# Kernel tuning notes

Measured on AMD Instinct MI355X. Metric: run time of the kernel, lower is better.

Reference implementation:

```python
import jax, jax.numpy as jnp
import numpy as np
from jax import lax

HIDDEN_CH = 32
KS = 3


def _conv(x, w):
    # x: [B, Cin, H, W], w: [Cout, Cin, k, k] -> [B, Cout, H, W] (SAME padding)
    return lax.conv_general_dilated(
        x, w, window_strides=(1, 1), padding='SAME',
        dimension_numbers=('NCHW', 'OIHW', 'NCHW'))


def _cell(x, h, gw, gb, cw, cb):
    combined = jnp.concatenate([x, h], axis=1)
    gates = jax.nn.sigmoid(_conv(combined, gw) + gb[None, :, None, None])
    r, z = jnp.split(gates, 2, axis=1)
    combined_r = jnp.concatenate([x, r * h], axis=1)
    n = jnp.tanh(_conv(combined_r, cw) + cb[None, :, None, None])
    return (1.0 - z) * h + z * n


def setup_inputs() -> dict:
    key = jax.random.key(0)
    ks = jax.random.split(key, 9)
    B, T, H, W = 8, 16, 128, 128
    hc = HIDDEN_CH
    seq = jax.random.normal(ks[0], (B, T, H, W), dtype=jnp.float32)

    def conv_init(k, cout, cin):
        fan_in = cin * KS * KS
        bound = 1.0 / np.sqrt(fan_in)
        return jax.random.uniform(k, (cout, cin, KS, KS), jnp.float32, -bound, bound)

    def bias_init(k, cout, cin):
        bound = 1.0 / np.sqrt(cin * KS * KS)
        return jax.random.uniform(k, (cout,), jnp.float32, -bound, bound)

    # Layer 0: input_ch=1, layer 1: input_ch=hc
    gw0 = conv_init(ks[1], 2 * hc, 1 + hc)
    gb0 = bias_init(ks[2], 2 * hc, 1 + hc)
    cw0 = conv_init(ks[3], hc, 1 + hc)
    cb0 = bias_init(ks[4], hc, 1 + hc)
    gw1 = conv_init(ks[5], 2 * hc, hc + hc)
    gb1 = bias_init(ks[6], 2 * hc, hc + hc)
    cw1 = conv_init(ks[7], hc, hc + hc)
    cb1 = bias_init(ks[8], hc, hc + hc)
    return {'seq': seq, 'gw0': gw0, 'gb0': gb0, 'cw0': cw0, 'cb0': cb0,
            'gw1': gw1, 'gb1': gb1, 'cw1': cw1, 'cb1': cb1}


def reference(seq, gw0, gb0, cw0, cb0, gw1, gb1, cw1, cb1):
    B, T, H, W = seq.shape
    hc = HIDDEN_CH
    h0 = jnp.zeros((B, hc, H, W), dtype=seq.dtype)
    h1 = jnp.zeros((B, hc, H, W), dtype=seq.dtype)
    # xs: [T, B, 1, H, W]
    xs = jnp.transpose(seq, (1, 0, 2, 3))[:, :, None, :, :]

    def step(carry, x_t):
        h0, h1 = carry
        h0 = _cell(x_t, h0, gw0, gb0, cw0, cb0)
        h1 = _cell(h0, h1, gw1, gb1, cw1, cb1)
        return (h0, h1), None

    (h0, h1), _ = lax.scan(step, (h0, h1), xs)
    return h1
```

## Files before the change

### kernel.cpp

```cpp
#include <hip/hip_runtime.h>


#define HH 128
#define PH 130
#define HW 16384
#define BB 8
#define TT 16

typedef _Float16 f16x8 __attribute__((ext_vector_type(8)));
typedef float f32x4 __attribute__((ext_vector_type(4)));
typedef unsigned int u32x4 __attribute__((ext_vector_type(4)));

__device__ __forceinline__ unsigned short f2h(float x){
    return __builtin_bit_cast(unsigned short, (_Float16)x);
}
__device__ __forceinline__ float h2f(unsigned short u){
    return (float)__builtin_bit_cast(_Float16, u);
}
__device__ __forceinline__ f16x8 ld_frag(const unsigned short* p){
    u32x4 v = *(const u32x4*)p;
    return __builtin_bit_cast(f16x8, v);
}
__device__ __forceinline__ f16x8 lds_frag_w(const unsigned short* base, int spix, int q){
    u32x4 v = *(const u32x4*)(base + spix * 32 + q * 8);
    return __builtin_bit_cast(f16x8, v);
}
__device__ __forceinline__ float sigmoid_f(float a){ return 1.0f / (1.0f + __expf(-a)); }
__device__ __forceinline__ float tanh_f(float a){ float e2 = __expf(2.0f * a); return 1.0f - 2.0f / (e2 + 1.0f); }

struct SmemT {
    unsigned short hs[2][13824];
    unsigned short rh[10880];
    float xt[444];
};

__device__ __forceinline__ void halo_rc10(int s, int& gr, int& gc){
    s = s > 83 ? 83 : s;
    if (s < 34)      { gr = 0;            gc = s;      }
    else if (s < 68) { gr = 9;            gc = s - 34; }
    else if (s < 76) { gr = 1 + (s - 68); gc = 0;      }
    else             { gr = 1 + (s - 76); gc = 33;     }
}

__device__ __forceinline__ f16x8 x_im2col(const float* xt, int gr, int gc, int q){
    f16x8 v;
#pragma unroll
    for (int j = 0; j < 8; ++j) {
        int k = q * 8 + j;
        float f = 0.0f;
        if (k < 9) f = xt[(gr + k / 3) * 37 + gc + k % 3];
        v[j] = (_Float16)f;
    }
    return v;
}

__device__ __forceinline__ void stage_plane12(unsigned short* slot,
    const unsigned short* __restrict__ g, int b, int pr0, int pc0)
{
    const int wv = threadIdx.x >> 6, lane = threadIdx.x & 63;
    for (int k = wv; k < 27; k += 8) {
        int chunk = k * 64 + lane;
        int pix = chunk >> 2, part = chunk & 3;
        int r = pix / 36, c = pix - r * 36;
        int pr = pr0 + r; pr = pr < 0 ? 0 : (pr > 129 ? 129 : pr);
        int pc = pc0 + c; pc = pc < 0 ? 0 : (pc > 129 ? 129 : pc);
        const unsigned short* ga = g + ((long)((b * PH + pr) * PH + pc) * 32 + part * 8);
        __builtin_amdgcn_global_load_lds(
            (const __attribute__((address_space(1))) unsigned int*)ga,
            (__attribute__((address_space(3))) unsigned int*)(slot + k * 512),
            16, 0, 0);
    }
}

__device__ __forceinline__ void stage_x12(float* xt, const float* __restrict__ seq,
                                          int b, int t, int R0, int C0)
{
    if (threadIdx.x < 444) {
        int p = threadIdx.x;
        int r = p / 37, c = p - r * 37;
        int ir = R0 - 2 + r, ic = C0 - 2 + c;
        float v = 0.0f;
        if (ir >= 0 && ir < HH && ic >= 0 && ic < HH)
            v = seq[((long)b * TT + t) * HW + ir * HH + ic];
        xt[p] = v;
    }
}

__global__ void prep_w(const float* __restrict__ w, unsigned short* __restrict__ wf,
                       int CO, int CIT, int NSTEP, int xmode)
{
    int idx = blockIdx.x * 256 + threadIdx.x;
    int total = NSTEP * CO * 32;
    if (idx >= total) return;
    int kk = idx & 31;
    int t  = idx >> 5;
    int co = t % CO;
    int s  = t / CO;
    float v = 0.0f;
    if (xmode && s == NSTEP - 1) {
        if (kk < 9) v = w[(co * CIT + 0) * 9 + kk];
    } else {
        int tap = s % 9;
        int cin = (s / 9) * 32 + kk + (xmode ? 1 : 0);
        v = w[(co * CIT + cin) * 9 + tap];
    }
    wf[idx] = f2h(v);
}

template<int L, int EMIT>
__device__ __forceinline__ void cell_compute(SmemT& sm,
    unsigned short* __restrict__ Hout,
    const unsigned short* __restrict__ Wg, const float* __restrict__ bg,
    const unsigned short* __restrict__ Wc, const float* __restrict__ bc,
    float* __restrict__ out, int b, int R0, int C0)
{
    constexpr int KG = (L == 0) ? 10 : 18;
    constexpr int KC = (L == 0) ? 10 : 18;

    const int wv = threadIdx.x >> 6, lane = threadIdx.x & 63;
    const int m16 = lane & 15, q = lane >> 4;
    const unsigned short* hp = (L == 0) ? sm.hs[0] : sm.hs[1];

    const bool HASH = (wv >= 2);
    int hgr = 0, hgc = 0;
    halo_rc10((wv - 2) * 16 + m16, hgr, hgc);

    f32x4 gI[2][4];
    f32x4 gH[2];
#pragma unroll
    for (int ng = 0; ng < 4; ++ng) {
        float bv = bg[ng * 16 + m16];
#pragma unroll
        for (int mg = 0; mg < 2; ++mg) gI[mg][ng] = f32x4{bv, bv, bv, bv};
        if (ng < 2) gH[ng] = f32x4{bv, bv, bv, bv};
    }

    f16x8 Bc[4];
#pragma unroll
    for (int ng = 0; ng < 4; ++ng)
        Bc[ng] = ld_frag(Wg + (ng * 16 + m16) * 32 + q * 8);

#pragma unroll
    for (int s = 0; s < KG; ++s) {
        f16x8 Bn[4];
        if (s + 1 < KG) {
#pragma unroll
            for (int ng = 0; ng < 4; ++ng)
                Bn[ng] = ld_frag(Wg + ((s + 1) * 64 + ng * 16 + m16) * 32 + q * 8);
        }
        f16x8 AI[2], AH;
        if (L == 0 && s == 9) {
#pragma unroll
            for (int mg = 0; mg < 2; ++mg)
                AI[mg] = x_im2col(sm.xt, wv + 1, mg * 16 + 1 + m16, q);
            AH = x_im2col(sm.xt, hgr, hgc, q);
        } else {
            const int tap = (L == 0) ? s : (s % 9);
            const unsigned short* pl = (L == 1 && s >= 9) ? sm.hs[1] : sm.hs[0];
#pragma unroll
            for (int mg = 0; mg < 2; ++mg)
                AI[mg] = lds_frag_w(pl, (wv + 1 + tap / 3) * 36 + mg * 16 + 1 + m16 + tap % 3, q);
            AH = lds_frag_w(pl, (hgr + tap / 3) * 36 + hgc + tap % 3, q);
        }
#pragma unroll
        for (int mg = 0; mg < 2; ++mg)
#pragma unroll
            for (int ng = 0; ng < 4; ++ng)
                gI[mg][ng] = __builtin_amdgcn_mfma_f32_16x16x32_f16(AI[mg], Bc[ng], gI[mg][ng], 0, 0, 0);
        if (HASH) {
#pragma unroll
            for (int ng = 0; ng < 2; ++ng)
                gH[ng] = __builtin_amdgcn_mfma_f32_16x16x32_f16(AH, Bc[ng], gH[ng], 0, 0, 0);
        }
        if (s + 1 < KG) {
#pragma unroll
            for (int ng = 0; ng < 4; ++ng) Bc[ng] = Bn[ng];
        }
    }

    unsigned int zpk[2][4];
#pragma unroll
    for (int mg = 0; mg < 2; ++mg)
#pragma unroll
        for (int rg = 0; rg < 4; ++rg) {
            int gr = wv + 1, gc = mg * 16 + 1 + q * 4 + rg;
            zpk[mg][rg] = (unsigned int)f2h(sigmoid_f(gI[mg][2][rg]))
                        | ((unsigned int)f2h(sigmoid_f(gI[mg][3][rg])) << 16);
#pragma unroll
            for (int ng = 0; ng < 2; ++ng) {
                int n = ng * 16 + m16;
                float rv = sigmoid_f(gI[mg][ng][rg]);
                float hv = h2f(hp[((gr + 1) * 36 + gc + 1) * 32 + n]);
                sm.rh[(gr * 34 + gc) * 32 + n] = f2h(rv * hv);
            }
        }
    if (HASH) {
#pragma unroll
        for (int rg = 0; rg < 4; ++rg) {
            int gr, gc; halo_rc10((wv - 2) * 16 + q * 4 + rg, gr, gc);
#pragma unroll
            for (int ng = 0; ng < 2; ++ng) {
                int n = ng * 16 + m16;
                float rv = sigmoid_f(gH[ng][rg]);
                float hv = h2f(hp[((gr + 1) * 36 + gc + 1) * 32 + n]);
                sm.rh[(gr * 34 + gc) * 32 + n] = f2h(rv * hv);
            }
        }
    }
    __syncthreads();

    f32x4 cacc[2][2];
#pragma unroll
    for (int mg = 0; mg < 2; ++mg)
#pragma unroll
        for (int ng = 0; ng < 2; ++ng) {
            float bv = bc[ng * 16 + m16];
            cacc[mg][ng] = f32x4{bv, bv, bv, bv};
        }
    f16x8 Cc[2];
#pragma unroll
    for (int ng = 0; ng < 2; ++ng)
        Cc[ng] = ld_frag(Wc + (ng * 16 + m16) * 32 + q * 8);
#pragma unroll
    for (int s = 0; s < KC; ++s) {
        f16x8 Cn[2];
        if (s + 1 < KC) {
#pragma unroll
            for (int ng = 0; ng < 2; ++ng)
                Cn[ng] = ld_frag(Wc + ((s + 1) * 32 + ng * 16 + m16) * 32 + q * 8);
        }
        f16x8 A2[2];
        if (L == 0 && s == 9) {
#pragma unroll
            for (int mg = 0; mg < 2; ++mg)
                A2[mg] = x_im2col(sm.xt, wv + 1, mg * 16 + 1 + m16, q);
        } else if (L == 1 && s < 9) {
#pragma unroll
            for (int mg = 0; mg < 2; ++mg)
                A2[mg] = lds_frag_w(sm.hs[0], (wv + 1 + s / 3) * 36 + mg * 16 + m16 + 1 + s % 3, q);
        } else {
            const int tap = (L == 0) ? s : (s - 9);
#pragma unroll
            for (int mg = 0; mg < 2; ++mg)
                A2[mg] = lds_frag_w(sm.rh, (wv + tap / 3) * 34 + mg * 16 + m16 + tap % 3, q);
        }
#pragma unroll
        for (int mg = 0; mg < 2; ++mg)
#pragma unroll
            for (int ng = 0; ng < 2; ++ng)
                cacc[mg][ng] = __builtin_amdgcn_mfma_f32_16x16x32_f16(A2[mg], Cc[ng], cacc[mg][ng], 0, 0, 0);
        if (s + 1 < KC) {
#pragma unroll
            for (int ng = 0; ng < 2; ++ng) Cc[ng] = Cn[ng];
        }
    }

    unsigned short hvout[2][2][4];
#pragma unroll
    for (int mg = 0; mg < 2; ++mg)
#pragma unroll
        for (int ng = 0; ng < 2; ++ng)
#pragma unroll
            for (int rg = 0; rg < 4; ++rg) {
                int lcol = mg * 16 + q * 4 + rg;
                int n = ng * 16 + m16;
                float nv = tanh_f(cacc[mg][ng][rg]);
                float zz = h2f((unsigned short)(zpk[mg][rg] >> (ng * 16)));
                float ho = h2f(hp[((wv + 2) * 36 + lcol + 2) * 32 + n]);
                float hnew = (1.0f - zz) * ho + zz * nv;
                if (!EMIT) {
                    long psp = (long)(b * PH + R0 + wv + 1) * PH + (C0 + lcol + 1);
                    Hout[psp * 32 + n] = f2h(hnew);
                } else {
                    hvout[mg][ng][rg] = f2h(hnew);
                }
            }

    if (EMIT) {
        __syncthreads();
        unsigned short* scr = sm.rh;
#pragma unroll
        for (int mg = 0; mg < 2; ++mg)
#pragma unroll
            for (int ng = 0; ng < 2; ++ng)
#pragma unroll
                for (int rg = 0; rg < 4; ++rg)
                    scr[((wv * 32 + mg * 16 + q * 4 + rg) * 32) + ng * 16 + m16] = hvout[mg][ng][rg];
        __syncthreads();
        const int tid = threadIdx.x;
        const int rowid = tid >> 1, half = tid & 1;
        const int n = rowid >> 3, wr = rowid & 7;
        long obase = ((long)(b * 32 + n) * HH + (R0 + wr)) * HH + C0 + half * 16;
#pragma unroll
        for (int j = 0; j < 16; ++j)
            out[obase + j] = h2f(scr[(wr * 32 + half * 16 + j) * 32 + n]);
    }
}

__global__ __launch_bounds__(512, 4)
void cell_l0(const unsigned short* __restrict__ Hin, unsigned short* __restrict__ Hout,
             const float* __restrict__ seq, int t,
             const unsigned short* __restrict__ Wg, const float* __restrict__ bg,
             const unsigned short* __restrict__ Wc, const float* __restrict__ bc)
{
    __shared__ __align__(16) SmemT sm;
    const int wg = blockIdx.x;
    const int b = wg >> 6, tr = (wg >> 2) & 15, tc = wg & 3;
    const int R0 = tr * 8, C0 = tc * 32;
    stage_x12(sm.xt, seq, b, t, R0, C0);
    stage_plane12(sm.hs[0], Hin, b, R0 - 1, C0 - 1);
    __syncthreads();
    cell_compute<0, 0>(sm, Hout, Wg, bg, Wc, bc, (float*)0, b, R0, C0);
}

__global__ __launch_bounds__(512, 4)
void fused_pair(const unsigned short* __restrict__ h1r, unsigned short* __restrict__ h1w,
                const unsigned short* __restrict__ h0r, unsigned short* __restrict__ h0w,
                const float* __restrict__ seq, int tnext,
                const unsigned short* __restrict__ WG0, const float* __restrict__ gb0,
                const unsigned short* __restrict__ WC0, const float* __restrict__ cb0,
                const unsigned short* __restrict__ WG1, const float* __restrict__ gb1,
                const unsigned short* __restrict__ WC1, const float* __restrict__ cb1)
{
    __shared__ __align__(16) SmemT sm;
    const int wg = blockIdx.x;
    const int b = wg >> 6, tr = (wg >> 2) & 15, tc = wg & 3;
    const int R0 = tr * 8, C0 = tc * 32;
    stage_x12(sm.xt, seq, b, tnext, R0, C0);
    stage_plane12(sm.hs[0], h0r, b, R0 - 1, C0 - 1);
    stage_plane12(sm.hs[1], h1r, b, R0 - 1, C0 - 1);
    __syncthreads();
    cell_compute<1, 0>(sm, h1w, WG1, gb1, WC1, cb1, (float*)0, b, R0, C0);
    __syncthreads();
    cell_compute<0, 0>(sm, h0w, WG0, gb0, WC0, cb0, (float*)0, b, R0, C0);
}

__global__ __launch_bounds__(512, 4)
void cell_l1_emit(const unsigned short* __restrict__ Hin,
                  const unsigned short* __restrict__ Xin,
                  const unsigned short* __restrict__ Wg, const float* __restrict__ bg,
                  const unsigned short* __restrict__ Wc, const float* __restrict__ bc,
                  float* __restrict__ out)
{
    __shared__ __align__(16) SmemT sm;
    const int wg = blockIdx.x;
    const int b = wg >> 6, tr = (wg >> 2) & 15, tc = wg & 3;
    const int R0 = tr * 8, C0 = tc * 32;
    stage_plane12(sm.hs[0], Xin, b, R0 - 1, C0 - 1);
    stage_plane12(sm.hs[1], Hin, b, R0 - 1, C0 - 1);
    __syncthreads();
    cell_compute<1, 1>(sm, (unsigned short*)0, Wg, bg, Wc, bc, out, b, R0, C0);
}

extern "C" void kernel_launch(void* const* d_in, const int* in_sizes, int n_in,
                              void* d_out, int out_size, void* d_ws, size_t ws_size,
                              hipStream_t stream)
{
    const float* seq = (const float*)d_in[0];
    const float* gw0 = (const float*)d_in[1];
    const float* gb0 = (const float*)d_in[2];
    const float* cw0 = (const float*)d_in[3];
    const float* cb0 = (const float*)d_in[4];
    const float* gw1 = (const float*)d_in[5];
    const float* gb1 = (const float*)d_in[6];
    const float* cw1 = (const float*)d_in[7];
    const float* cb1 = (const float*)d_in[8];
    float* out = (float*)d_out;

    const size_t NSP = (size_t)BB * PH * PH * 32;

    char* p = (char*)d_ws;
    unsigned short* S0A = (unsigned short*)p; p += NSP * 2;
    unsigned short* S0B = (unsigned short*)p; p += NSP * 2;
    unsigned short* S1A = (unsigned short*)p; p += NSP * 2;
    unsigned short* S1B = (unsigned short*)p; p += NSP * 2;
    unsigned short* WG0 = (unsigned short*)p; p += 20480 * 2;
    unsigned short* WC0 = (unsigned short*)p; p += 10240 * 2;
    unsigned short* WG1 = (unsigned short*)p; p += 36864 * 2;
    unsigned short* WC1 = (unsigned short*)p; p += 18432 * 2;

    hipMemsetAsync(S0A, 0, 4 * NSP * 2, stream);

    prep_w<<<(10 * 64 * 32 + 255) / 256, 256, 0, stream>>>(gw0, WG0, 64, 33, 10, 1);
    prep_w<<<(10 * 32 * 32 + 255) / 256, 256, 0, stream>>>(cw0, WC0, 32, 33, 10, 1);
    prep_w<<<(18 * 64 * 32 + 255) / 256, 256, 0, stream>>>(gw1, WG1, 64, 64, 18, 0);
    prep_w<<<(18 * 32 * 32 + 255) / 256, 256, 0, stream>>>(cw1, WC1, 32, 64, 18, 0);

    dim3 grid(512, 1, 1), block(512);

    cell_l0<<<grid, block, 0, stream>>>(S0A, S0B, seq, 0, WG0, gb0, WC0, cb0);

    unsigned short *h0r = S0B, *h0w = S0A, *h1r = S1A, *h1w = S1B;
    for (int t = 0; t < TT - 1; ++t) {
        fused_pair<<<grid, block, 0, stream>>>(h1r, h1w, h0r, h0w, seq, t + 1,
                                               WG0, gb0, WC0, cb0,
                                               WG1, gb1, WC1, cb1);
        unsigned short* tmp;
        tmp = h0r; h0r = h0w; h0w = tmp;
        tmp = h1r; h1r = h1w; h1w = tmp;
    }
    cell_l1_emit<<<grid, block, 0, stream>>>(h1r, h0r, WG1, gb1, WC1, cb1, out);
}
```

Before: 1.005 ms.

## Split layer cells into separate blocks and swizzle LDS activation tiles

The fused per-step kernel used to run the layer-1 cell and then the layer-0 cell one after the other inside each block. It now launches a grid with a z dimension of 2, so one set of blocks computes layer 1 and another set computes layer 0 concurrently, doubling the number of blocks per launch. Separately, staged activation planes and the r*h buffer in shared memory now use an XOR swizzle on load and on every access, to reduce LDS bank conflicts on the 16-byte fragment reads. The layer-0 blocks now stage the h0 halo themselves, so the h0 plane is read twice from global memory.

```diff
diff --git a/kernel.cpp b/kernel.cpp
--- a/kernel.cpp
+++ b/kernel.cpp
@@ -21,8 +21,10 @@
     u32x4 v = *(const u32x4*)p;
     return __builtin_bit_cast(f16x8, v);
 }
-__device__ __forceinline__ f16x8 lds_frag_w(const unsigned short* base, int spix, int q){
-    u32x4 v = *(const u32x4*)(base + spix * 32 + q * 8);
+__device__ __forceinline__ int swzus(int i){ return i ^ (((i >> 6) & 7) << 3); }
+__device__ __forceinline__ f16x8 lds_frag_s(const unsigned short* base, int spix, int q){
+    int idx = swzus(spix * 32 + q * 8);
+    u32x4 v = *(const u32x4*)(base + idx);
     return __builtin_bit_cast(f16x8, v);
 }
 __device__ __forceinline__ float sigmoid_f(float a){ return 1.0f / (1.0f + __expf(-a)); }
@@ -59,8 +61,9 @@
 {
     const int wv = threadIdx.x >> 6, lane = threadIdx.x & 63;
     for (int k = wv; k < 27; k += 8) {
-        int chunk = k * 64 + lane;
-        int pix = chunk >> 2, part = chunk & 3;
+        int u = k * 64 + lane;
+        int cch = u ^ ((u >> 3) & 7);
+        int pix = cch >> 2, part = cch & 3;
         int r = pix / 36, c = pix - r * 36;
         int pr = pr0 + r; pr = pr < 0 ? 0 : (pr > 129 ? 129 : pr);
         int pc = pc0 + c; pc = pc < 0 ? 0 : (pc > 129 ? 129 : pc);
@@ -159,8 +162,8 @@
             const unsigned short* pl = (L == 1 && s >= 9) ? sm.hs[1] : sm.hs[0];
 #pragma unroll
             for (int mg = 0; mg < 2; ++mg)
-                AI[mg] = lds_frag_w(pl, (wv + 1 + tap / 3) * 36 + mg * 16 + 1 + m16 + tap % 3, q);
-            AH = lds_frag_w(pl, (hgr + tap / 3) * 36 + hgc + tap % 3, q);
+                AI[mg] = lds_frag_s(pl, (wv + 1 + tap / 3) * 36 + mg * 16 + 1 + m16 + tap % 3, q);
+            AH = lds_frag_s(pl, (hgr + tap / 3) * 36 + hgc + tap % 3, q);
         }
 #pragma unroll
         for (int mg = 0; mg < 2; ++mg)
@@ -190,8 +193,8 @@
             for (int ng = 0; ng < 2; ++ng) {
                 int n = ng * 16 + m16;
                 float rv = sigmoid_f(gI[mg][ng][rg]);
-                float hv = h2f(hp[((gr + 1) * 36 + gc + 1) * 32 + n]);
-                sm.rh[(gr * 34 + gc) * 32 + n] = f2h(rv * hv);
+                float hv = h2f(hp[swzus(((gr + 1) * 36 + gc + 1) * 32 + n)]);
+                sm.rh[swzus((gr * 34 + gc) * 32 + n)] = f2h(rv * hv);
             }
         }
     if (HASH) {
@@ -202,8 +205,8 @@
             for (int ng = 0; ng < 2; ++ng) {
                 int n = ng * 16 + m16;
                 float rv = sigmoid_f(gH[ng][rg]);
-                float hv = h2f(hp[((gr + 1) * 36 + gc + 1) * 32 + n]);
-                sm.rh[(gr * 34 + gc) * 32 + n] = f2h(rv * hv);
+                float hv = h2f(hp[swzus(((gr + 1) * 36 + gc + 1) * 32 + n)]);
+                sm.rh[swzus((gr * 34 + gc) * 32 + n)] = f2h(rv * hv);
             }
         }
     }
@@ -237,12 +240,12 @@
         } else if (L == 1 && s < 9) {
 #pragma unroll
             for (int mg = 0; mg < 2; ++mg)
-                A2[mg] = lds_frag_w(sm.hs[0], (wv + 1 + s / 3) * 36 + mg * 16 + m16 + 1 + s % 3, q);
+                A2[mg] = lds_frag_s(sm.hs[0], (wv + 1 + s / 3) * 36 + mg * 16 + m16 + 1 + s % 3, q);
         } else {
             const int tap = (L == 0) ? s : (s - 9);
 #pragma unroll
             for (int mg = 0; mg < 2; ++mg)
-                A2[mg] = lds_frag_w(sm.rh, (wv + tap / 3) * 34 + mg * 16 + m16 + tap % 3, q);
+                A2[mg] = lds_frag_s(sm.rh, (wv + tap / 3) * 34 + mg * 16 + m16 + tap % 3, q);
         }
 #pragma unroll
         for (int mg = 0; mg < 2; ++mg)
@@ -266,7 +269,7 @@
                 int n = ng * 16 + m16;
                 float nv = tanh_f(cacc[mg][ng][rg]);
                 float zz = h2f((unsigned short)(zpk[mg][rg] >> (ng * 16)));
-                float ho = h2f(hp[((wv + 2) * 36 + lcol + 2) * 32 + n]);
+                float ho = h2f(hp[swzus(((wv + 2) * 36 + lcol + 2) * 32 + n)]);
                 float hnew = (1.0f - zz) * ho + zz * nv;
                 if (!EMIT) {
                     long psp = (long)(b * PH + R0 + wv + 1) * PH + (C0 + lcol + 1);
@@ -314,25 +317,29 @@
 }
 
 __global__ __launch_bounds__(512, 4)
-void fused_pair(const unsigned short* __restrict__ h1r, unsigned short* __restrict__ h1w,
-                const unsigned short* __restrict__ h0r, unsigned short* __restrict__ h0w,
-                const float* __restrict__ seq, int tnext,
-                const unsigned short* __restrict__ WG0, const float* __restrict__ gb0,
-                const unsigned short* __restrict__ WC0, const float* __restrict__ cb0,
-                const unsigned short* __restrict__ WG1, const float* __restrict__ gb1,
-                const unsigned short* __restrict__ WC1, const float* __restrict__ cb1)
+void step_pair(const unsigned short* __restrict__ h1r, unsigned short* __restrict__ h1w,
+               const unsigned short* __restrict__ h0r, unsigned short* __restrict__ h0w,
+               const float* __restrict__ seq, int tnext,
+               const unsigned short* __restrict__ WG0, const float* __restrict__ gb0,
+               const unsigned short* __restrict__ WC0, const float* __restrict__ cb0,
+               const unsigned short* __restrict__ WG1, const float* __restrict__ gb1,
+               const unsigned short* __restrict__ WC1, const float* __restrict__ cb1)
 {
     __shared__ __align__(16) SmemT sm;
     const int wg = blockIdx.x;
     const int b = wg >> 6, tr = (wg >> 2) & 15, tc = wg & 3;
     const int R0 = tr * 8, C0 = tc * 32;
-    stage_x12(sm.xt, seq, b, tnext, R0, C0);
-    stage_plane12(sm.hs[0], h0r, b, R0 - 1, C0 - 1);
-    stage_plane12(sm.hs[1], h1r, b, R0 - 1, C0 - 1);
-    __syncthreads();
-    cell_compute<1, 0>(sm, h1w, WG1, gb1, WC1, cb1, (float*)0, b, R0, C0);
-    __syncthreads();
-    cell_compute<0, 0>(sm, h0w, WG0, gb0, WC0, cb0, (float*)0, b, R0, C0);
+    if (blockIdx.z == 0) {
+        stage_plane12(sm.hs[0], h0r, b, R0 - 1, C0 - 1);
+        stage_plane12(sm.hs[1], h1r, b, R0 - 1, C0 - 1);
+        __syncthreads();
+        cell_compute<1, 0>(sm, h1w, WG1, gb1, WC1, cb1, (float*)0, b, R0, C0);
+    } else {
+        stage_x12(sm.xt, seq, b, tnext, R0, C0);
+        stage_plane12(sm.hs[0], h0r, b, R0 - 1, C0 - 1);
+        __syncthreads();
+        cell_compute<0, 0>(sm, h0w, WG0, gb0, WC0, cb0, (float*)0, b, R0, C0);
+    }
 }
 
 __global__ __launch_bounds__(512, 4)
@@ -386,18 +393,18 @@
     prep_w<<<(18 * 64 * 32 + 255) / 256, 256, 0, stream>>>(gw1, WG1, 64, 64, 18, 0);
     prep_w<<<(18 * 32 * 32 + 255) / 256, 256, 0, stream>>>(cw1, WC1, 32, 64, 18, 0);
 
-    dim3 grid(512, 1, 1), block(512);
-
-    cell_l0<<<grid, block, 0, stream>>>(S0A, S0B, seq, 0, WG0, gb0, WC0, cb0);
+    dim3 grid1(512, 1, 1), grid2(512, 1, 2), block(512);
+
+    cell_l0<<<grid1, block, 0, stream>>>(S0A, S0B, seq, 0, WG0, gb0, WC0, cb0);
 
     unsigned short *h0r = S0B, *h0w = S0A, *h1r = S1A, *h1w = S1B;
     for (int t = 0; t < TT - 1; ++t) {
-        fused_pair<<<grid, block, 0, stream>>>(h1r, h1w, h0r, h0w, seq, t + 1,
+        step_pair<<<grid2, block, 0, stream>>>(h1r, h1w, h0r, h0w, seq, t + 1,
                                                WG0, gb0, WC0, cb0,
                                                WG1, gb1, WC1, cb1);
         unsigned short* tmp;
         tmp = h0r; h0r = h0w; h0w = tmp;
         tmp = h1r; h1r = h1w; h1w = tmp;
     }
-    cell_l1_emit<<<grid, block, 0, stream>>>(h1r, h0r, WG1, gb1, WC1, cb1, out);
-}
+    cell_l1_emit<<<grid1, block, 0, stream>>>(h1r, h0r, WG1, gb1, WC1, cb1, out);
+}
```

After: 1.004 ms. Within noise of the previous version (-0.1%).

## Split layer cells across blockIdx.z and pack output channel pairs

Applied to the files above, without the earlier changes.

The fused per-step kernel used to run layer 1 and then layer 0 one after the other inside each workgroup. It now launches twice as many workgroups, and blockIdx.z picks which layer's cell a block computes, so the two cells run in parallel. Output channels are permuted in the weight prep and bias indexing so each lane owns adjacent channel pairs. This allows 32-bit packed LDS and global loads and stores for h, r*h and the new hidden state. Weight fragment loads are hoisted ahead of a barrier placed inside cell_compute, which overlaps them with staging. The cost is that h0 staging is duplicated across the two block groups, and the workgroup count doubles.

```diff
diff --git a/kernel.cpp b/kernel.cpp
--- a/kernel.cpp
+++ b/kernel.cpp
@@ -27,6 +27,9 @@
 }
 __device__ __forceinline__ float sigmoid_f(float a){ return 1.0f / (1.0f + __expf(-a)); }
 __device__ __forceinline__ float tanh_f(float a){ float e2 = __expf(2.0f * a); return 1.0f - 2.0f / (e2 + 1.0f); }
+__device__ __forceinline__ unsigned int packh2(float lo, float hi){
+    return (unsigned int)f2h(lo) | ((unsigned int)f2h(hi) << 16);
+}
 
 struct SmemT {
     unsigned short hs[2][13824];
@@ -96,13 +99,14 @@
     int t  = idx >> 5;
     int co = t % CO;
     int s  = t / CO;
+    int lco = (co & ~31) | (2 * (co & 15) + ((co >> 4) & 1));
     float v = 0.0f;
     if (xmode && s == NSTEP - 1) {
-        if (kk < 9) v = w[(co * CIT + 0) * 9 + kk];
+        if (kk < 9) v = w[(lco * CIT + 0) * 9 + kk];
     } else {
         int tap = s % 9;
         int cin = (s / 9) * 32 + kk + (xmode ? 1 : 0);
-        v = w[(co * CIT + cin) * 9 + tap];
+        v = w[(lco * CIT + cin) * 9 + tap];
     }
     wf[idx] = f2h(v);
 }
@@ -121,6 +125,17 @@
     const int m16 = lane & 15, q = lane >> 4;
     const unsigned short* hp = (L == 0) ? sm.hs[0] : sm.hs[1];
 
+    f16x8 Bc[4];
+#pragma unroll
+    for (int ng = 0; ng < 4; ++ng)
+        Bc[ng] = ld_frag(Wg + (ng * 16 + m16) * 32 + q * 8);
+    f16x8 Cc[2];
+#pragma unroll
+    for (int ng = 0; ng < 2; ++ng)
+        Cc[ng] = ld_frag(Wc + (ng * 16 + m16) * 32 + q * 8);
+
+    __syncthreads();
+
     const bool HASH = (wv >= 2);
     int hgr = 0, hgc = 0;
     halo_rc10((wv - 2) * 16 + m16, hgr, hgc);
@@ -129,16 +144,11 @@
     f32x4 gH[2];
 #pragma unroll
     for (int ng = 0; ng < 4; ++ng) {
-        float bv = bg[ng * 16 + m16];
+        float bv = bg[(ng >> 1) * 32 + 2 * m16 + (ng & 1)];
 #pragma unroll
         for (int mg = 0; mg < 2; ++mg) gI[mg][ng] = f32x4{bv, bv, bv, bv};
         if (ng < 2) gH[ng] = f32x4{bv, bv, bv, bv};
     }
-
-    f16x8 Bc[4];
-#pragma unroll
-    for (int ng = 0; ng < 4; ++ng)
-        Bc[ng] = ld_frag(Wg + (ng * 16 + m16) * 32 + q * 8);
 
 #pragma unroll
     for (int s = 0; s < KG; ++s) {
@@ -184,27 +194,22 @@
 #pragma unroll
         for (int rg = 0; rg < 4; ++rg) {
             int gr = wv + 1, gc = mg * 16 + 1 + q * 4 + rg;
-            zpk[mg][rg] = (unsigned int)f2h(sigmoid_f(gI[mg][2][rg]))
-                        | ((unsigned int)f2h(sigmoid_f(gI[mg][3][rg])) << 16);
-#pragma unroll
-            for (int ng = 0; ng < 2; ++ng) {
-                int n = ng * 16 + m16;
-                float rv = sigmoid_f(gI[mg][ng][rg]);
-                float hv = h2f(hp[((gr + 1) * 36 + gc + 1) * 32 + n]);
-                sm.rh[(gr * 34 + gc) * 32 + n] = f2h(rv * hv);
-            }
+            zpk[mg][rg] = packh2(sigmoid_f(gI[mg][2][rg]), sigmoid_f(gI[mg][3][rg]));
+            float rv0 = sigmoid_f(gI[mg][0][rg]);
+            float rv1 = sigmoid_f(gI[mg][1][rg]);
+            unsigned int hvp = *(const unsigned int*)(hp + ((gr + 1) * 36 + gc + 1) * 32 + 2 * m16);
+            float h0 = h2f((unsigned short)hvp), h1 = h2f((unsigned short)(hvp >> 16));
+            *(unsigned int*)(sm.rh + (gr * 34 + gc) * 32 + 2 * m16) = packh2(rv0 * h0, rv1 * h1);
         }
     if (HASH) {
 #pragma unroll
         for (int rg = 0; rg < 4; ++rg) {
             int gr, gc; halo_rc10((wv - 2) * 16 + q * 4 + rg, gr, gc);
-#pragma unroll
-            for (int ng = 0; ng < 2; ++ng) {
-                int n = ng * 16 + m16;
-                float rv = sigmoid_f(gH[ng][rg]);
-                float hv = h2f(hp[((gr + 1) * 36 + gc + 1) * 32 + n]);
-                sm.rh[(gr * 34 + gc) * 32 + n] = f2h(rv * hv);
-            }
+            float rv0 = sigmoid_f(gH[0][rg]);
+            float rv1 = sigmoid_f(gH[1][rg]);
+            unsigned int hvp = *(const unsigned int*)(hp + ((gr + 1) * 36 + gc + 1) * 32 + 2 * m16);
+            float h0 = h2f((unsigned short)hvp), h1 = h2f((unsigned short)(hvp >> 16));
+            *(unsigned int*)(sm.rh + (gr * 34 + gc) * 32 + 2 * m16) = packh2(rv0 * h0, rv1 * h1);
         }
     }
     __syncthreads();
@@ -214,13 +219,9 @@
     for (int mg = 0; mg < 2; ++mg)
 #pragma unroll
         for (int ng = 0; ng < 2; ++ng) {
-            float bv = bc[ng * 16 + m16];
+            float bv = bc[2 * m16 + ng];
             cacc[mg][ng] = f32x4{bv, bv, bv, bv};
         }
-    f16x8 Cc[2];
-#pragma unroll
-    for (int ng = 0; ng < 2; ++ng)
-        Cc[ng] = ld_frag(Wc + (ng * 16 + m16) * 32 + q * 8);
 #pragma unroll
     for (int s = 0; s < KC; ++s) {
         f16x8 Cn[2];
@@ -255,26 +256,27 @@
         }
     }
 
-    unsigned short hvout[2][2][4];
+    unsigned int hvout[2][4];
 #pragma unroll
     for (int mg = 0; mg < 2; ++mg)
 #pragma unroll
-        for (int ng = 0; ng < 2; ++ng)
-#pragma unroll
-            for (int rg = 0; rg < 4; ++rg) {
-                int lcol = mg * 16 + q * 4 + rg;
-                int n = ng * 16 + m16;
-                float nv = tanh_f(cacc[mg][ng][rg]);
-                float zz = h2f((unsigned short)(zpk[mg][rg] >> (ng * 16)));
-                float ho = h2f(hp[((wv + 2) * 36 + lcol + 2) * 32 + n]);
-                float hnew = (1.0f - zz) * ho + zz * nv;
-                if (!EMIT) {
-                    long psp = (long)(b * PH + R0 + wv + 1) * PH + (C0 + lcol + 1);
-                    Hout[psp * 32 + n] = f2h(hnew);
-                } else {
-                    hvout[mg][ng][rg] = f2h(hnew);
-                }
+        for (int rg = 0; rg < 4; ++rg) {
+            int lcol = mg * 16 + q * 4 + rg;
+            float nv0 = tanh_f(cacc[mg][0][rg]);
+            float nv1 = tanh_f(cacc[mg][1][rg]);
+            float zz0 = h2f((unsigned short)zpk[mg][rg]);
+            float zz1 = h2f((unsigned short)(zpk[mg][rg] >> 16));
+            unsigned int hop = *(const unsigned int*)(hp + ((wv + 2) * 36 + lcol + 2) * 32 + 2 * m16);
+            float ho0 = h2f((unsigned short)hop), ho1 = h2f((unsigned short)(hop >> 16));
+            float hn0 = (1.0f - zz0) * ho0 + zz0 * nv0;
+            float hn1 = (1.0f - zz1) * ho1 + zz1 * nv1;
+            if (!EMIT) {
+                long psp = (long)(b * PH + R0 + wv + 1) * PH + (C0 + lcol + 1);
+                *(unsigned int*)(Hout + psp * 32 + 2 * m16) = packh2(hn0, hn1);
+            } else {
+                hvout[mg][rg] = packh2(hn0, hn1);
             }
+        }
 
     if (EMIT) {
         __syncthreads();
@@ -282,10 +284,9 @@
 #pragma unroll
         for (int mg = 0; mg < 2; ++mg)
 #pragma unroll
-            for (int ng = 0; ng < 2; ++ng)
-#pragma unroll
-                for (int rg = 0; rg < 4; ++rg)
-                    scr[((wv * 32 + mg * 16 + q * 4 + rg) * 32) + ng * 16 + m16] = hvout[mg][ng][rg];
+            for (int rg = 0; rg < 4; ++rg)
+                *(unsigned int*)(scr + ((wv * 32 + mg * 16 + q * 4 + rg) * 32) + 2 * m16)
+                    = hvout[mg][rg];
         __syncthreads();
         const int tid = threadIdx.x;
         const int rowid = tid >> 1, half = tid & 1;
@@ -309,30 +310,31 @@
     const int R0 = tr * 8, C0 = tc * 32;
     stage_x12(sm.xt, seq, b, t, R0, C0);
     stage_plane12(sm.hs[0], Hin, b, R0 - 1, C0 - 1);
-    __syncthreads();
     cell_compute<0, 0>(sm, Hout, Wg, bg, Wc, bc, (float*)0, b, R0, C0);
 }
 
 __global__ __launch_bounds__(512, 4)
-void fused_pair(const unsigned short* __restrict__ h1r, unsigned short* __restrict__ h1w,
-                const unsigned short* __restrict__ h0r, unsigned short* __restrict__ h0w,
-                const float* __restrict__ seq, int tnext,
-                const unsigned short* __restrict__ WG0, const float* __restrict__ gb0,
-                const unsigned short* __restrict__ WC0, const float* __restrict__ cb0,
-                const unsigned short* __restrict__ WG1, const float* __restrict__ gb1,
-                const unsigned short* __restrict__ WC1, const float* __restrict__ cb1)
+void step_pair(const unsigned short* __restrict__ h1r, unsigned short* __restrict__ h1w,
+               const unsigned short* __restrict__ h0r, unsigned short* __restrict__ h0w,
+               const float* __restrict__ seq, int tnext,
+               const unsigned short* __restrict__ WG0, const float* __restrict__ gb0,
+               const unsigned short* __restrict__ WC0, const float* __restrict__ cb0,
+               const unsigned short* __restrict__ WG1, const float* __restrict__ gb1,
+               const unsigned short* __restrict__ WC1, const float* __restrict__ cb1)
 {
     __shared__ __align__(16) SmemT sm;
     const int wg = blockIdx.x;
     const int b = wg >> 6, tr = (wg >> 2) & 15, tc = wg & 3;
     const int R0 = tr * 8, C0 = tc * 32;
-    stage_x12(sm.xt, seq, b, tnext, R0, C0);
-    stage_plane12(sm.hs[0], h0r, b, R0 - 1, C0 - 1);
-    stage_plane12(sm.hs[1], h1r, b, R0 - 1, C0 - 1);
-    __syncthreads();
-    cell_compute<1, 0>(sm, h1w, WG1, gb1, WC1, cb1, (float*)0, b, R0, C0);
-    __syncthreads();
-    cell_compute<0, 0>(sm, h0w, WG0, gb0, WC0, cb0, (float*)0, b, R0, C0);
+    if (blockIdx.z == 0) {
+        stage_plane12(sm.hs[0], h0r, b, R0 - 1, C0 - 1);
+        stage_plane12(sm.hs[1], h1r, b, R0 - 1, C0 - 1);
+        cell_compute<1, 0>(sm, h1w, WG1, gb1, WC1, cb1, (float*)0, b, R0, C0);
+    } else {
+        stage_x12(sm.xt, seq, b, tnext, R0, C0);
+        stage_plane12(sm.hs[0], h0r, b, R0 - 1, C0 - 1);
+        cell_compute<0, 0>(sm, h0w, WG0, gb0, WC0, cb0, (float*)0, b, R0, C0);
+    }
 }
 
 __global__ __launch_bounds__(512, 4)
@@ -348,7 +350,6 @@
     const int R0 = tr * 8, C0 = tc * 32;
     stage_plane12(sm.hs[0], Xin, b, R0 - 1, C0 - 1);
     stage_plane12(sm.hs[1], Hin, b, R0 - 1, C0 - 1);
-    __syncthreads();
     cell_compute<1, 1>(sm, (unsigned short*)0, Wg, bg, Wc, bc, out, b, R0, C0);
 }
 
@@ -386,18 +387,18 @@
     prep_w<<<(18 * 64 * 32 + 255) / 256, 256, 0, stream>>>(gw1, WG1, 64, 64, 18, 0);
     prep_w<<<(18 * 32 * 32 + 255) / 256, 256, 0, stream>>>(cw1, WC1, 32, 64, 18, 0);
 
-    dim3 grid(512, 1, 1), block(512);
-
-    cell_l0<<<grid, block, 0, stream>>>(S0A, S0B, seq, 0, WG0, gb0, WC0, cb0);
+    dim3 grid1(512, 1, 1), grid2(512, 1, 2), block(512);
+
+    cell_l0<<<grid1, block, 0, stream>>>(S0A, S0B, seq, 0, WG0, gb0, WC0, cb0);
 
     unsigned short *h0r = S0B, *h0w = S0A, *h1r = S1A, *h1w = S1B;
     for (int t = 0; t < TT - 1; ++t) {
-        fused_pair<<<grid, block, 0, stream>>>(h1r, h1w, h0r, h0w, seq, t + 1,
+        step_pair<<<grid2, block, 0, stream>>>(h1r, h1w, h0r, h0w, seq, t + 1,
                                                WG0, gb0, WC0, cb0,
                                                WG1, gb1, WC1, cb1);
         unsigned short* tmp;
         tmp = h0r; h0r = h0w; h0w = tmp;
         tmp = h1r; h1r = h1w; h1w = tmp;
     }
-    cell_l1_emit<<<grid, block, 0, stream>>>(h1r, h0r, WG1, gb1, WC1, cb1, out);
-}
+    cell_l1_emit<<<grid1, block, 0, stream>>>(h1r, h0r, WG1, gb1, WC1, cb1, out);
+}
```

New measurement: 972.9 us. 1.03x faster.
